# Optimization experiments

Measured on AMD Instinct MI355X. Metric: run time of the kernel, lower is better.

The kernel has to match this reference:

```python
import jax, jax.numpy as jnp
import numpy as np

B, S, D_IN, D_OUT = 4, 2048, 1024, 1024


def setup_inputs() -> dict:
    key = jax.random.key(0)
    ks = jax.random.split(key, 7)
    s_in = 1.0 / np.sqrt(D_IN)
    return {
        "x": jax.random.normal(ks[0], (B, S, D_IN), dtype=jnp.float32),
        "Wq": jax.random.uniform(ks[1], (D_IN, D_OUT), jnp.float32, -s_in, s_in),
        "bq": jax.random.uniform(ks[2], (D_OUT,), jnp.float32, -s_in, s_in),
        "Wk": jax.random.uniform(ks[3], (D_IN, D_OUT), jnp.float32, -s_in, s_in),
        "bk": jax.random.uniform(ks[4], (D_OUT,), jnp.float32, -s_in, s_in),
        "Wv": jax.random.uniform(ks[5], (D_IN, D_OUT), jnp.float32, -s_in, s_in),
        "bv": jax.random.uniform(ks[6], (D_OUT,), jnp.float32, -s_in, s_in),
    }


def reference(x, Wq, bq, Wk, bk, Wv, bv):
    # Linear projections (torch Linear: x @ W^T + b; here W stored as [in,out])
    q = x @ Wq + bq  # [B,S,D]
    k = x @ Wk + bk
    v = x @ Wv + bv
    scores = jnp.einsum("bqd,bkd->bqk", q, k)  # [B,S,S]
    # causal mask: positions j > i masked with -inf (applied BEFORE scaling,
    # which is equivalent since -inf/sqrt(d) == -inf)
    seq = scores.shape[-1]
    causal = jnp.tril(jnp.ones((seq, seq), dtype=bool))
    masked = jnp.where(causal, scores, -jnp.inf)
    attn = jax.nn.softmax(masked / np.sqrt(k.shape[-1]), axis=-1)
    # dropout p=0.0 -> identity
    return attn @ v  # [B,S,D]
```

## Files before the change

kernel.cpp:

```cpp
#include <hip/hip_runtime.h>

typedef unsigned short u16;
typedef unsigned int u32;
typedef __attribute__((ext_vector_type(8))) short short8;
typedef __attribute__((ext_vector_type(4))) float f32x4;

__device__ __forceinline__ u16 f2bf(float f) {
    u32 u = __float_as_uint(f);
    u32 r = (u + 0x7fffu + ((u >> 16) & 1u)) >> 16;
    return (u16)r;
}
__device__ __forceinline__ float bf2f(u16 h) {
    return __uint_as_float(((u32)h) << 16);
}

__device__ __forceinline__ void gld16(u16* lds_dst, const u16* g_src) {
    __builtin_amdgcn_global_load_lds(
        (const __attribute__((address_space(1))) unsigned int*)g_src,
        (__attribute__((address_space(3))) unsigned int*)lds_dst,
        16, 0, 0);
}

__global__ void split_x_k(const float* __restrict__ x, u16* __restrict__ xh,
                          u16* __restrict__ xl) {
    long i = ((long)blockIdx.x * 256 + threadIdx.x) * 4;
    float4 f = *(const float4*)(x + i);
    u16 h0 = f2bf(f.x), h1 = f2bf(f.y), h2 = f2bf(f.z), h3 = f2bf(f.w);
    u16 l0 = f2bf(f.x - bf2f(h0)), l1 = f2bf(f.y - bf2f(h1));
    u16 l2 = f2bf(f.z - bf2f(h2)), l3 = f2bf(f.w - bf2f(h3));
    uint2 hv, lv;
    hv.x = (u32)h0 | ((u32)h1 << 16); hv.y = (u32)h2 | ((u32)h3 << 16);
    lv.x = (u32)l0 | ((u32)l1 << 16); lv.y = (u32)l2 | ((u32)l3 << 16);
    *(uint2*)(xh + i) = hv;
    *(uint2*)(xl + i) = lv;
}

__global__ void splitT_w_k(const float* __restrict__ Wq, const float* __restrict__ Wk,
                           const float* __restrict__ Wv, u16* __restrict__ wth,
                           u16* __restrict__ wtl) {
    __shared__ float tile[32][33];
    int z = blockIdx.z;
    const float* W = (z == 0) ? Wq : (z == 1) ? Wk : Wv;
    int n0 = blockIdx.x * 32, k0 = blockIdx.y * 32;
    int tx = threadIdx.x, ty = threadIdx.y;
#pragma unroll
    for (int r0 = 0; r0 < 4; ++r0) {
        int r = ty + r0 * 8;
        tile[r][tx] = W[(long)(k0 + r) * 1024 + n0 + tx];
    }
    __syncthreads();
    long zoff = (long)z * 1024 * 1024;
#pragma unroll
    for (int r0 = 0; r0 < 4; ++r0) {
        int r = ty + r0 * 8;
        float f = tile[tx][r];
        u16 h = f2bf(f), l = f2bf(f - bf2f(h));
        long idx = zoff + (long)(n0 + r) * 1024 + k0 + tx;
        wth[idx] = h;
        wtl[idx] = l;
    }
}

__global__ void transpose_v_k(const u16* __restrict__ vh, const u16* __restrict__ vl,
                              u16* __restrict__ vth, u16* __restrict__ vtl) {
    __shared__ u16 th[32][33];
    __shared__ u16 tl[32][33];
    int z = blockIdx.z;
    int d0 = blockIdx.x * 32, s0 = blockIdx.y * 32;
    int tx = threadIdx.x, ty = threadIdx.y;
#pragma unroll
    for (int r0 = 0; r0 < 4; ++r0) {
        int r = ty + r0 * 8;
        long idx = ((long)z * 2048 + s0 + r) * 1024 + d0 + tx;
        th[r][tx] = vh[idx];
        tl[r][tx] = vl[idx];
    }
    __syncthreads();
    long zoff = (long)z * 1024 * 2048;
#pragma unroll
    for (int r0 = 0; r0 < 4; ++r0) {
        int r = ty + r0 * 8;
        long idx = zoff + (long)(d0 + r) * 2048 + s0 + tx;
        vth[idx] = th[tx][r];
        vtl[idx] = tl[tx][r];
    }
}

__launch_bounds__(512, 2)
__global__ void proj_k(const u16* __restrict__ Ah, const u16* __restrict__ Al,
                       const u16* __restrict__ Bh, const u16* __restrict__ Bl,
                       u16* __restrict__ oh, u16* __restrict__ ol,
                       const float* __restrict__ bias) {
    constexpr int NF = 4;
    constexpr int BN = 256;
    constexpr int SLOT = 8192 + NF * 4096;
    __shared__ u16 lds[3 * SLOT];

    const int bi = blockIdx.x, bj = blockIdx.y;
    const int nsteps = 32;

    const int tid = threadIdx.x;
    const int lane = tid & 63, w = tid >> 6;
    const int wr = w >> 2, wc = w & 3;

    const int srow = tid >> 2;
    const int ls8 = (((tid & 3) ^ ((tid >> 3) & 3)) << 3);
    const long aoff  = ((long)bi * 128 + srow) * 1024 + ls8;
    const long boff0 = ((long)bj * BN + srow) * 1024 + ls8;
    const long boff1 = boff0 + 128L * 1024;
    const int wbase = w * 512;

    f32x4 acc[4][NF] = {};

    const int fr = lane & 15;
    const int ps8 = (((lane >> 4) ^ ((fr >> 1) & 3)) << 3);

    auto stage = [&](int slot, int step) {
        const int k0 = step * 32;
        u16* sb = lds + slot * SLOT;
        gld16(sb + wbase,               Ah + aoff + k0);
        gld16(sb + 4096 + wbase,        Al + aoff + k0);
        gld16(sb + 8192 + wbase,        Bh + boff0 + k0);
        gld16(sb + 12288 + wbase,       Bh + boff1 + k0);
        gld16(sb + 16384 + wbase,       Bl + boff0 + k0);
        gld16(sb + 20480 + wbase,       Bl + boff1 + k0);
    };

    auto compute = [&](int slot) {
        const u16* LA = lds + slot * SLOT;
        const u16* LB = LA + 8192;
        short8 afh[4], afl[4], bfh[NF], bfl[NF];
#pragma unroll
        for (int m = 0; m < 4; ++m) {
            int off = (wr * 64 + m * 16 + fr) * 32 + ps8;
            afh[m] = *(const short8*)(LA + off);
            afl[m] = *(const short8*)(LA + 4096 + off);
        }
#pragma unroll
        for (int n = 0; n < NF; ++n) {
            int off = (wc * (NF * 16) + n * 16 + fr) * 32 + ps8;
            bfh[n] = *(const short8*)(LB + off);
            bfl[n] = *(const short8*)(LB + NF * 2048 + off);
        }
        __builtin_amdgcn_s_setprio(1);
#pragma unroll
        for (int m = 0; m < 4; ++m)
#pragma unroll
            for (int n = 0; n < NF; ++n) {
                acc[m][n] = __builtin_amdgcn_mfma_f32_16x16x32_bf16(afh[m], bfh[n], acc[m][n], 0, 0, 0);
                acc[m][n] = __builtin_amdgcn_mfma_f32_16x16x32_bf16(afh[m], bfl[n], acc[m][n], 0, 0, 0);
                acc[m][n] = __builtin_amdgcn_mfma_f32_16x16x32_bf16(afl[m], bfh[n], acc[m][n], 0, 0, 0);
            }
        __builtin_amdgcn_s_setprio(0);
    };

    stage(0, 0);
    stage(1, 1);
    int cs = 0, ns = 2;
    for (int h = 0; h < nsteps; ++h) {
        if (h + 1 < nsteps) {
            asm volatile("s_waitcnt vmcnt(6)" ::: "memory");
        } else {
            asm volatile("s_waitcnt vmcnt(0)" ::: "memory");
        }
        __builtin_amdgcn_s_barrier();
        __builtin_amdgcn_sched_barrier(0);
        if (h + 2 < nsteps) stage(ns, h + 2);
        compute(cs);
        cs = (cs == 2) ? 0 : cs + 1;
        ns = (ns == 2) ? 0 : ns + 1;
    }

    const int row0 = bi * 128 + wr * 64 + (lane >> 4) * 4;
    const int col0 = bj * BN + wc * (NF * 16) + (lane & 15);
#pragma unroll
    for (int n = 0; n < NF; ++n) {
        float bv = bias[col0 + n * 16];
#pragma unroll
        for (int m = 0; m < 4; ++m)
#pragma unroll
            for (int j = 0; j < 4; ++j) {
                float v = acc[m][n][j] + bv;
                long idx = (long)(row0 + m * 16 + j) * 1024 + col0 + n * 16;
                u16 h = f2bf(v);
                oh[idx] = h;
                ol[idx] = f2bf(v - bf2f(h));
            }
    }
}

__launch_bounds__(512, 2)
__global__ void qk_k(const u16* __restrict__ Qh, const u16* __restrict__ Ql,
                     const u16* __restrict__ Kh, const u16* __restrict__ Kl,
                     float* __restrict__ S) {
    constexpr int SLOT = 16384;
    __shared__ u16 lds[2 * SLOT];

    const int bi = blockIdx.x, bj = blockIdx.y, z = blockIdx.z;
    if (bj > bi) return;
    const int nsteps = 32;

    const u16* gA_h = Qh + (long)z * 2048 * 1024;
    const u16* gA_l = Ql + (long)z * 2048 * 1024;
    const u16* gB_h = Kh + (long)z * 2048 * 1024;
    const u16* gB_l = Kl + (long)z * 2048 * 1024;

    const int tid = threadIdx.x;
    const int lane = tid & 63, w = tid >> 6;
    const int wr = w >> 2, wc = w & 3;

    const int srow = tid >> 2;
    const int ls8 = (((tid & 3) ^ ((tid >> 3) & 3)) << 3);
    const long aoff  = ((long)bi * 128 + srow) * 1024 + ls8;
    const long boff0 = ((long)bj * 128 + srow) * 1024 + ls8;
    const int wbase = w * 512;

    f32x4 acc[4][2] = {};
    const int fr = lane & 15;
    const int ps8 = (((lane >> 4) ^ ((fr >> 1) & 3)) << 3);

    auto stage = [&](int slot, int step) {
        const int k0 = step * 32;
        u16* sb = lds + slot * SLOT;
        gld16(sb + wbase,         gA_h + aoff + k0);
        gld16(sb + 4096 + wbase,  gA_l + aoff + k0);
        gld16(sb + 8192 + wbase,  gB_h + boff0 + k0);
        gld16(sb + 12288 + wbase, gB_l + boff0 + k0);
    };

    auto compute = [&](int slot) {
        const u16* LA = lds + slot * SLOT;
        const u16* LB = LA + 8192;
        short8 afh[4], afl[4], bfh[2], bfl[2];
#pragma unroll
        for (int m = 0; m < 4; ++m) {
            int off = (wr * 64 + m * 16 + fr) * 32 + ps8;
            afh[m] = *(const short8*)(LA + off);
            afl[m] = *(const short8*)(LA + 4096 + off);
        }
#pragma unroll
        for (int n = 0; n < 2; ++n) {
            int off = (wc * 32 + n * 16 + fr) * 32 + ps8;
            bfh[n] = *(const short8*)(LB + off);
            bfl[n] = *(const short8*)(LB + 4096 + off);
        }
        __builtin_amdgcn_s_setprio(1);
#pragma unroll
        for (int m = 0; m < 4; ++m)
#pragma unroll
            for (int n = 0; n < 2; ++n) {
                acc[m][n] = __builtin_amdgcn_mfma_f32_16x16x32_bf16(afh[m], bfh[n], acc[m][n], 0, 0, 0);
                acc[m][n] = __builtin_amdgcn_mfma_f32_16x16x32_bf16(afh[m], bfl[n], acc[m][n], 0, 0, 0);
                acc[m][n] = __builtin_amdgcn_mfma_f32_16x16x32_bf16(afl[m], bfh[n], acc[m][n], 0, 0, 0);
            }
        __builtin_amdgcn_s_setprio(0);
    };

    stage(0, 0);
    int cs = 0;
    for (int h = 0; h < nsteps; ++h) {
        asm volatile("s_waitcnt vmcnt(0)" ::: "memory");
        __builtin_amdgcn_s_barrier();
        __builtin_amdgcn_sched_barrier(0);
        if (h + 1 < nsteps) stage(cs ^ 1, h + 1);
        compute(cs);
        cs ^= 1;
    }

    const int row0 = bi * 128 + wr * 64 + (lane >> 4) * 4;
    const int col0 = bj * 128 + wc * 32 + (lane & 15);
    float* o = S + (long)z * 2048 * 2048;
#pragma unroll
    for (int m = 0; m < 4; ++m)
#pragma unroll
        for (int n = 0; n < 2; ++n)
#pragma unroll
            for (int j = 0; j < 4; ++j)
                o[(long)(row0 + m * 16 + j) * 2048 + col0 + n * 16] = acc[m][n][j];
}

__global__ void softmax_k(const float* __restrict__ S, u16* __restrict__ Ph,
                          u16* __restrict__ Pl) {
    const long row = blockIdx.x;
    const int i = (int)(row & 2047);
    const float* srow = S + row * 2048;
    u16* ph = Ph + row * 2048;
    u16* pl = Pl + row * 2048;
    const int t = threadIdx.x;
    const int limit = ((i >> 7) + 1) << 7;

    float v[8];
    float m = -1e30f;
#pragma unroll
    for (int j = 0; j < 8; ++j) {
        int c = j * 256 + t;
        float x = (c <= i) ? srow[c] : -1e30f;
        v[j] = x;
        m = fmaxf(m, x);
    }
#pragma unroll
    for (int off = 32; off; off >>= 1) m = fmaxf(m, __shfl_xor(m, off));
    __shared__ float redm[4], reds[4];
    if ((t & 63) == 0) redm[t >> 6] = m;
    __syncthreads();
    m = fmaxf(fmaxf(redm[0], redm[1]), fmaxf(redm[2], redm[3]));

    float p[8];
    float s = 0.f;
#pragma unroll
    for (int j = 0; j < 8; ++j) {
        int c = j * 256 + t;
        float e = (c <= i) ? __expf((v[j] - m) * 0.03125f) : 0.f;
        p[j] = e;
        s += e;
    }
#pragma unroll
    for (int off = 32; off; off >>= 1) s += __shfl_xor(s, off);
    if ((t & 63) == 0) reds[t >> 6] = s;
    __syncthreads();
    s = reds[0] + reds[1] + reds[2] + reds[3];
    const float inv = 1.f / s;
#pragma unroll
    for (int j = 0; j < 8; ++j) {
        int c = j * 256 + t;
        if (c < limit) {
            float o = p[j] * inv;
            u16 h = f2bf(o);
            ph[c] = h;
            pl[c] = f2bf(o - bf2f(h));
        }
    }
}

__launch_bounds__(512, 2)
__global__ void pv_k(const u16* __restrict__ Ph, const u16* __restrict__ Pl,
                     const u16* __restrict__ Vth, const u16* __restrict__ Vtl,
                     float* __restrict__ out) {
    constexpr int SLOT = 16384;
    __shared__ u16 lds[2 * SLOT];

    const int bi = 15 - (int)blockIdx.x;
    const int bj = blockIdx.y, z = blockIdx.z;
    const int nsteps = (bi + 1) * 4;

    const u16* gA_h = Ph + (long)z * 2048 * 2048;
    const u16* gA_l = Pl + (long)z * 2048 * 2048;
    const u16* gB_h = Vth + (long)z * 1024 * 2048;
    const u16* gB_l = Vtl + (long)z * 1024 * 2048;

    const int tid = threadIdx.x;
    const int lane = tid & 63, w = tid >> 6;
    const int wr = w >> 2, wc = w & 3;

    const int srow = tid >> 2;
    const int ls8 = (((tid & 3) ^ ((tid >> 3) & 3)) << 3);
    const long aoff  = ((long)bi * 128 + srow) * 2048 + ls8;
    const long boff0 = ((long)bj * 128 + srow) * 2048 + ls8;
    const int wbase = w * 512;

    f32x4 acc[4][2] = {};
    const int fr = lane & 15;
    const int ps8 = (((lane >> 4) ^ ((fr >> 1) & 3)) << 3);

    auto stage = [&](int slot, int step) {
        const int k0 = step * 32;
        u16* sb = lds + slot * SLOT;
        gld16(sb + wbase,         gA_h + aoff + k0);
        gld16(sb + 4096 + wbase,  gA_l + aoff + k0);
        gld16(sb + 8192 + wbase,  gB_h + boff0 + k0);
        gld16(sb + 12288 + wbase, gB_l + boff0 + k0);
    };

    auto compute = [&](int slot) {
        const u16* LA = lds + slot * SLOT;
        const u16* LB = LA + 8192;
        short8 afh[4], afl[4], bfh[2], bfl[2];
#pragma unroll
        for (int m = 0; m < 4; ++m) {
            int off = (wr * 64 + m * 16 + fr) * 32 + ps8;
            afh[m] = *(const short8*)(LA + off);
            afl[m] = *(const short8*)(LA + 4096 + off);
        }
#pragma unroll
        for (int n = 0; n < 2; ++n) {
            int off = (wc * 32 + n * 16 + fr) * 32 + ps8;
            bfh[n] = *(const short8*)(LB + off);
            bfl[n] = *(const short8*)(LB + 4096 + off);
        }
        __builtin_amdgcn_s_setprio(1);
#pragma unroll
        for (int m = 0; m < 4; ++m)
#pragma unroll
            for (int n = 0; n < 2; ++n) {
                acc[m][n] = __builtin_amdgcn_mfma_f32_16x16x32_bf16(afh[m], bfh[n], acc[m][n], 0, 0, 0);
                acc[m][n] = __builtin_amdgcn_mfma_f32_16x16x32_bf16(afh[m], bfl[n], acc[m][n], 0, 0, 0);
                acc[m][n] = __builtin_amdgcn_mfma_f32_16x16x32_bf16(afl[m], bfh[n], acc[m][n], 0, 0, 0);
            }
        __builtin_amdgcn_s_setprio(0);
    };

    stage(0, 0);
    int cs = 0;
    for (int h = 0; h < nsteps; ++h) {
        asm volatile("s_waitcnt vmcnt(0)" ::: "memory");
        __builtin_amdgcn_s_barrier();
        __builtin_amdgcn_sched_barrier(0);
        if (h + 1 < nsteps) stage(cs ^ 1, h + 1);
        compute(cs);
        cs ^= 1;
    }

    const int row0 = bi * 128 + wr * 64 + (lane >> 4) * 4;
    const int col0 = bj * 128 + wc * 32 + (lane & 15);
    float* o = out + (long)z * 2048 * 1024;
#pragma unroll
    for (int m = 0; m < 4; ++m)
#pragma unroll
        for (int n = 0; n < 2; ++n)
#pragma unroll
            for (int j = 0; j < 4; ++j)
                o[(long)(row0 + m * 16 + j) * 1024 + col0 + n * 16] = acc[m][n][j];
}

extern "C" void kernel_launch(void* const* d_in, const int* in_sizes, int n_in,
                              void* d_out, int out_size, void* d_ws, size_t ws_size,
                              hipStream_t stream) {
    const float* x  = (const float*)d_in[0];
    const float* Wq = (const float*)d_in[1];
    const float* bq = (const float*)d_in[2];
    const float* Wk = (const float*)d_in[3];
    const float* bk = (const float*)d_in[4];
    const float* Wv = (const float*)d_in[5];
    const float* bv = (const float*)d_in[6];
    float* out = (float*)d_out;
    char* ws = (char*)d_ws;
    const size_t MB = 1ull << 20;

    u16* xs_hi = (u16*)(ws + 0 * MB);
    u16* xs_lo = (u16*)(ws + 16 * MB);
    u16* wt_hi = (u16*)(ws + 32 * MB);
    u16* wt_lo = (u16*)(ws + 38 * MB);
    float* S   = (float*)(ws + 0 * MB);
    u16* q_hi = (u16*)(ws + 64 * MB);
    u16* q_lo = (u16*)(ws + 80 * MB);
    u16* k_hi = (u16*)(ws + 96 * MB);
    u16* k_lo = (u16*)(ws + 112 * MB);
    u16* P_hi = (u16*)(ws + 64 * MB);
    u16* P_lo = (u16*)(ws + 96 * MB);
    u16* v_hi  = (u16*)(ws + 128 * MB);
    u16* v_lo  = (u16*)(ws + 144 * MB);
    u16* vt_hi = (u16*)(ws + 160 * MB);
    u16* vt_lo = (u16*)(ws + 176 * MB);

    const long WZ = 1024L * 1024;

    split_x_k<<<8192, 256, 0, stream>>>(x, xs_hi, xs_lo);
    splitT_w_k<<<dim3(32, 32, 3), dim3(32, 8), 0, stream>>>(Wq, Wk, Wv, wt_hi, wt_lo);
    proj_k<<<dim3(64, 4), 512, 0, stream>>>(xs_hi, xs_lo, wt_hi,          wt_lo,          q_hi, q_lo, bq);
    proj_k<<<dim3(64, 4), 512, 0, stream>>>(xs_hi, xs_lo, wt_hi + WZ,     wt_lo + WZ,     k_hi, k_lo, bk);
    proj_k<<<dim3(64, 4), 512, 0, stream>>>(xs_hi, xs_lo, wt_hi + 2 * WZ, wt_lo + 2 * WZ, v_hi, v_lo, bv);
    transpose_v_k<<<dim3(32, 64, 4), dim3(32, 8), 0, stream>>>(v_hi, v_lo, vt_hi, vt_lo);
    qk_k<<<dim3(16, 16, 4), 512, 0, stream>>>(q_hi, q_lo, k_hi, k_lo, S);
    softmax_k<<<8192, 256, 0, stream>>>(S, P_hi, P_lo);
    pv_k<<<dim3(16, 8, 4), 512, 0, stream>>>(P_hi, P_lo, vt_hi, vt_lo, out);
}
```

Before: 460.2 us.

## Merge Q/K/V projections into one launch and rebalance causal block scheduling

The three projection launches become a single 3D grid, with blockIdx.z selecting the weight slice, bias and output buffers. This removes two launch gaps and lets all projection blocks fill the GPU together. The qk and pv kernels now use a flattened grid, remapped so each group of blocks mixes short and long causal rows (bi and 15-bi) across batches, and so consecutive block IDs are spread across XCDs. The aim is better load balance in the triangular work, at the cost of more complex index arithmetic and possibly different cache locality.

```diff
diff --git a/kernel.cpp b/kernel.cpp
--- a/kernel.cpp
+++ b/kernel.cpp
@@ -89,15 +89,22 @@
 __launch_bounds__(512, 2)
 __global__ void proj_k(const u16* __restrict__ Ah, const u16* __restrict__ Al,
                        const u16* __restrict__ Bh, const u16* __restrict__ Bl,
-                       u16* __restrict__ oh, u16* __restrict__ ol,
-                       const float* __restrict__ bias) {
+                       u16* __restrict__ oh0, u16* __restrict__ oh1, u16* __restrict__ oh2,
+                       u16* __restrict__ ol0, u16* __restrict__ ol1, u16* __restrict__ ol2,
+                       const float* __restrict__ b0, const float* __restrict__ b1,
+                       const float* __restrict__ b2) {
     constexpr int NF = 4;
     constexpr int BN = 256;
     constexpr int SLOT = 8192 + NF * 4096;
     __shared__ u16 lds[3 * SLOT];
 
-    const int bi = blockIdx.x, bj = blockIdx.y;
+    const int bi = blockIdx.x, bj = blockIdx.y, z = blockIdx.z;
     const int nsteps = 32;
+
+    const u16* gA_h = Ah;
+    const u16* gA_l = Al;
+    const u16* gB_h = Bh + (long)z * 1024 * 1024;
+    const u16* gB_l = Bl + (long)z * 1024 * 1024;
 
     const int tid = threadIdx.x;
     const int lane = tid & 63, w = tid >> 6;
@@ -118,12 +125,12 @@
     auto stage = [&](int slot, int step) {
         const int k0 = step * 32;
         u16* sb = lds + slot * SLOT;
-        gld16(sb + wbase,               Ah + aoff + k0);
-        gld16(sb + 4096 + wbase,        Al + aoff + k0);
-        gld16(sb + 8192 + wbase,        Bh + boff0 + k0);
-        gld16(sb + 12288 + wbase,       Bh + boff1 + k0);
-        gld16(sb + 16384 + wbase,       Bl + boff0 + k0);
-        gld16(sb + 20480 + wbase,       Bl + boff1 + k0);
+        gld16(sb + wbase,               gA_h + aoff + k0);
+        gld16(sb + 4096 + wbase,        gA_l + aoff + k0);
+        gld16(sb + 8192 + wbase,        gB_h + boff0 + k0);
+        gld16(sb + 12288 + wbase,       gB_h + boff1 + k0);
+        gld16(sb + 16384 + wbase,       gB_l + boff0 + k0);
+        gld16(sb + 20480 + wbase,       gB_l + boff1 + k0);
     };
 
     auto compute = [&](int slot) {
@@ -173,6 +180,10 @@
 
     const int row0 = bi * 128 + wr * 64 + (lane >> 4) * 4;
     const int col0 = bj * BN + wc * (NF * 16) + (lane & 15);
+
+    const float* bias = (z == 0) ? b0 : (z == 1) ? b1 : b2;
+    u16* oh = (z == 0) ? oh0 : (z == 1) ? oh1 : oh2;
+    u16* ol = (z == 0) ? ol0 : (z == 1) ? ol1 : ol2;
 #pragma unroll
     for (int n = 0; n < NF; ++n) {
         float bv = bias[col0 + n * 16];
@@ -196,7 +207,13 @@
     constexpr int SLOT = 16384;
     __shared__ u16 lds[2 * SLOT];
 
-    const int bi = blockIdx.x, bj = blockIdx.y, z = blockIdx.z;
+    const int bid = blockIdx.x;
+    const int logical = (bid & 7) * 128 + (bid >> 3);
+    const int bj = logical & 15;
+    const int gidx = logical >> 4;
+    const int c = gidx >> 3, j = gidx & 7;
+    const int bi = (j < 4) ? c : 15 - c;
+    const int z = j & 3;
     if (bj > bi) return;
     const int nsteps = 32;
 
@@ -339,8 +356,13 @@
     constexpr int SLOT = 16384;
     __shared__ u16 lds[2 * SLOT];
 
-    const int bi = 15 - (int)blockIdx.x;
-    const int bj = blockIdx.y, z = blockIdx.z;
+    const int bid = blockIdx.x;
+    const int logical = (bid & 7) * 64 + (bid >> 3);
+    const int bj = logical & 7;
+    const int gidx = logical >> 3;
+    const int c = gidx >> 3, j = gidx & 7;
+    const int bi = (j < 4) ? c : 15 - c;
+    const int z = j & 3;
     const int nsteps = (bi + 1) * 4;
 
     const u16* gA_h = Ph + (long)z * 2048 * 2048;
@@ -452,15 +474,12 @@
     u16* vt_hi = (u16*)(ws + 160 * MB);
     u16* vt_lo = (u16*)(ws + 176 * MB);
 
-    const long WZ = 1024L * 1024;
-
     split_x_k<<<8192, 256, 0, stream>>>(x, xs_hi, xs_lo);
     splitT_w_k<<<dim3(32, 32, 3), dim3(32, 8), 0, stream>>>(Wq, Wk, Wv, wt_hi, wt_lo);
-    proj_k<<<dim3(64, 4), 512, 0, stream>>>(xs_hi, xs_lo, wt_hi,          wt_lo,          q_hi, q_lo, bq);
-    proj_k<<<dim3(64, 4), 512, 0, stream>>>(xs_hi, xs_lo, wt_hi + WZ,     wt_lo + WZ,     k_hi, k_lo, bk);
-    proj_k<<<dim3(64, 4), 512, 0, stream>>>(xs_hi, xs_lo, wt_hi + 2 * WZ, wt_lo + 2 * WZ, v_hi, v_lo, bv);
+    proj_k<<<dim3(64, 4, 3), 512, 0, stream>>>(
+        xs_hi, xs_lo, wt_hi, wt_lo, q_hi, k_hi, v_hi, q_lo, k_lo, v_lo, bq, bk, bv);
     transpose_v_k<<<dim3(32, 64, 4), dim3(32, 8), 0, stream>>>(v_hi, v_lo, vt_hi, vt_lo);
-    qk_k<<<dim3(16, 16, 4), 512, 0, stream>>>(q_hi, q_lo, k_hi, k_lo, S);
+    qk_k<<<1024, 512, 0, stream>>>(q_hi, q_lo, k_hi, k_lo, S);
     softmax_k<<<8192, 256, 0, stream>>>(S, P_hi, P_lo);
-    pv_k<<<dim3(16, 8, 4), 512, 0, stream>>>(P_hi, P_lo, vt_hi, vt_lo, out);
-}
+    pv_k<<<512, 512, 0, stream>>>(P_hi, P_lo, vt_hi, vt_lo, out);
+}
```

Result: faster. 408.8 us (-11.2%).
